# Kernel optimization log

Measured on AMD Instinct MI355X. Metric: run time of the kernel, lower is better.

## Reference

```python
import jax, jax.numpy as jnp
import numpy as np

N_NODES = 100000
N_EDGES = 1600000
IN_C, HID_C, OUT_C = 128, 64, 32


def gcn_conv(x, W, b, src, dst, n_nodes):
    """PyG GCNConv with default add_self_loops=True, symmetric normalization.

    out_i = sum_{j->i} (deg_j^-1/2 * deg_i^-1/2) * (x_j @ W) + (1/deg_i) * (x_i @ W) + b
    where deg counts incoming edges plus the self-loop.
    """
    h = x @ W  # [N, F_out] -- transform first (F_out <= F_in), cheaper messages
    # degree at target nodes, including self-loop weight 1
    deg = jax.ops.segment_sum(jnp.ones(src.shape[0], dtype=h.dtype), dst,
                              num_segments=n_nodes) + 1.0
    dinv = jax.lax.rsqrt(deg)  # deg >= 1 always (self-loop)
    # edge messages with symmetric norm, scattered to destination nodes
    coef = dinv[src] * dinv[dst]  # [E]
    msg = h[src] * coef[:, None]  # [E, F_out]
    agg = jax.ops.segment_sum(msg, dst, num_segments=n_nodes)
    # self-loop contribution: norm = dinv_i * dinv_i = 1/deg_i
    agg = agg + h * (dinv * dinv)[:, None]
    return agg + b


def setup_inputs() -> dict:
    key = jax.random.key(0)
    ks = jax.random.split(key, 8)
    x = jax.random.normal(ks[0], (N_NODES, IN_C), dtype=jnp.float32)
    edge_index = jax.random.randint(ks[1], (2, N_EDGES), 0, N_NODES, dtype=jnp.int64)
    s0 = 1.0 / np.sqrt(IN_C)
    s1 = 1.0 / np.sqrt(HID_C)
    W0 = jax.random.uniform(ks[2], (IN_C, HID_C), jnp.float32, -s0, s0)
    b0 = jnp.zeros((HID_C,), jnp.float32)
    Wm = jax.random.uniform(ks[3], (HID_C, OUT_C), jnp.float32, -s1, s1)
    bm = jnp.zeros((OUT_C,), jnp.float32)
    Wl = jax.random.uniform(ks[4], (HID_C, OUT_C), jnp.float32, -s1, s1)
    bl = jnp.zeros((OUT_C,), jnp.float32)
    return {"x": x, "edge_index": edge_index, "W0": W0, "b0": b0,
            "Wm": Wm, "bm": bm, "Wl": Wl, "bl": bl}


def reference(x, edge_index, W0, b0, Wm, bm, Wl, bl):
    src, dst = edge_index[0], edge_index[1]
    n = x.shape[0]
    h = gcn_conv(x, W0, b0, src, dst, n)
    h = jax.nn.relu(h)
    mean = gcn_conv(h, Wm, bm, src, dst, n)
    logstd = gcn_conv(h, Wl, bl, src, dst, n)
    return (mean, logstd)
```

## Files before the change

### kernel.cpp

```cpp
#include <hip/hip_runtime.h>
#include <hip/hip_fp16.h>


__global__ void hist_rank_kernel(const int* __restrict__ dst, int E, int* __restrict__ count,
                                 int* __restrict__ rank) {
    int stride = gridDim.x * blockDim.x;
    int t = blockIdx.x * blockDim.x + threadIdx.x;
    int E4 = E >> 2;
    for (int e = t; e < E4; e += stride) {
        int4 d = ((const int4*)dst)[e];
        int4 r;
        r.x = atomicAdd(&count[d.x], 1);
        r.y = atomicAdd(&count[d.y], 1);
        r.z = atomicAdd(&count[d.z], 1);
        r.w = atomicAdd(&count[d.w], 1);
        ((int4*)rank)[e] = r;
    }
    for (int e = (E4 << 2) + t; e < E; e += stride) rank[e] = atomicAdd(&count[dst[e]], 1);
}

__global__ void scan_partial_kernel(const int* __restrict__ count, int* __restrict__ partials,
                                    int N) {
    __shared__ int red[4];
    int t = threadIdx.x;
    int idx = blockIdx.x * 1024 + t * 4;
    int s = 0;
    if (idx + 3 < N) {
        int4 c = *(const int4*)(count + idx);
        s = c.x + c.y + c.z + c.w;
    } else {
#pragma unroll
        for (int k = 0; k < 4; ++k)
            if (idx + k < N) s += count[idx + k];
    }
#pragma unroll
    for (int off = 1; off < 64; off <<= 1) s += __shfl_xor(s, off);
    if ((t & 63) == 0) red[t >> 6] = s;
    __syncthreads();
    if (t == 0) partials[blockIdx.x] = red[0] + red[1] + red[2] + red[3];
}

__global__ void scan_top_kernel(int* __restrict__ partials, int nb, int* __restrict__ row_ptr,
                                int N) {
    __shared__ int buf[2][128];
    int t = threadIdx.x;
    buf[0][t] = (t < nb) ? partials[t] : 0;
    __syncthreads();
    int pi = 0;
    for (int off = 1; off < 128; off <<= 1) {
        int v = buf[pi][t];
        if (t >= off) v += buf[pi][t - off];
        buf[pi ^ 1][t] = v;
        pi ^= 1;
        __syncthreads();
    }
    if (t < nb) partials[t] = (t == 0) ? 0 : buf[pi][t - 1];
    if (t == 0) row_ptr[N] = buf[pi][127];
}

__global__ void scan_apply_kernel(const int* __restrict__ count, const int* __restrict__ partials,
                                  int* __restrict__ row_ptr, float* __restrict__ dinv, int N) {
    __shared__ int wsum[4];
    int t = threadIdx.x;
    int idx = blockIdx.x * 1024 + t * 4;
    int4 c = make_int4(0, 0, 0, 0);
    if (idx + 3 < N) {
        c = *(const int4*)(count + idx);
    } else {
        if (idx + 0 < N) c.x = count[idx + 0];
        if (idx + 1 < N) c.y = count[idx + 1];
        if (idx + 2 < N) c.z = count[idx + 2];
    }
    int s = c.x + c.y + c.z + c.w;
    int incl = s;
#pragma unroll
    for (int off = 1; off < 64; off <<= 1) {
        int v = __shfl_up(incl, off);
        if ((t & 63) >= off) incl += v;
    }
    int wexcl = incl - s;
    int w = t >> 6;
    if ((t & 63) == 63) wsum[w] = incl;
    __syncthreads();
    int base = partials[blockIdx.x] + wexcl;
    for (int k = 0; k < w; ++k) base += wsum[k];
    if (idx + 0 < N) { row_ptr[idx + 0] = base;                   dinv[idx + 0] = rsqrtf((float)c.x + 1.f); }
    if (idx + 1 < N) { row_ptr[idx + 1] = base + c.x;             dinv[idx + 1] = rsqrtf((float)c.y + 1.f); }
    if (idx + 2 < N) { row_ptr[idx + 2] = base + c.x + c.y;       dinv[idx + 2] = rsqrtf((float)c.z + 1.f); }
    if (idx + 3 < N) { row_ptr[idx + 3] = base + c.x + c.y + c.z; dinv[idx + 3] = rsqrtf((float)c.w + 1.f); }
}

#define NPASS 8
__global__ void scatter_kernel(const int* __restrict__ src, const int* __restrict__ dst,
                               const int* __restrict__ rank, int E,
                               const int* __restrict__ row_ptr, int* __restrict__ col, int N) {
    int chunk = (N + NPASS - 1) / NPASS;
    int stride = gridDim.x * blockDim.x;
    int t = blockIdx.x * blockDim.x + threadIdx.x;
    int E4 = E >> 2;
    for (int pass = 0; pass < NPASS; ++pass) {
        int lo = pass * chunk, hi = min(lo + chunk, N);
        for (int e = t; e < E4; e += stride) {
            int4 d = ((const int4*)dst)[e];
            int4 s = ((const int4*)src)[e];
            int4 r = ((const int4*)rank)[e];
            if (d.x >= lo && d.x < hi) col[row_ptr[d.x] + r.x] = s.x;
            if (d.y >= lo && d.y < hi) col[row_ptr[d.y] + r.y] = s.y;
            if (d.z >= lo && d.z < hi) col[row_ptr[d.z] + r.z] = s.z;
            if (d.w >= lo && d.w < hi) col[row_ptr[d.w] + r.w] = s.w;
        }
        for (int e = (E4 << 2) + t; e < E; e += stride) {
            int d = dst[e];
            if (d >= lo && d < hi) col[row_ptr[d] + rank[e]] = src[e];
        }
    }
}


__global__ __launch_bounds__(256, 2) void gemm_kernel(const float* __restrict__ A,
                                                      const float* __restrict__ W,
                                                      const float* __restrict__ dinv,
                                                      __half* __restrict__ Out, int M) {
    const int K = 128;
    __shared__ float Ws[K][64];
    __shared__ float As[64][68];
    int t = threadIdx.x;
    for (int i = t * 4; i < K * 64; i += 1024)
        *(float4*)&Ws[i >> 6][i & 63] = *(const float4*)(W + i);

    int row0 = blockIdx.x * 64;
    int rt = (t >> 4) * 4;
    int ct = (t & 15) * 4;
    float acc[4][4];
#pragma unroll
    for (int m = 0; m < 4; m++) { acc[m][0] = 0.f; acc[m][1] = 0.f; acc[m][2] = 0.f; acc[m][3] = 0.f; }

    for (int k0 = 0; k0 < K; k0 += 64) {
        __syncthreads();
        for (int i = t * 4; i < 64 * 64; i += 1024) {
            int r = i >> 6, c = i & 63;
            int gr = row0 + r;
            float4 v = make_float4(0.f, 0.f, 0.f, 0.f);
            if (gr < M) v = *(const float4*)(A + (size_t)gr * K + k0 + c);
            *(float4*)&As[r][c] = v;
        }
        __syncthreads();
#pragma unroll
        for (int kk = 0; kk < 64; ++kk) {
            float a0 = As[rt + 0][kk], a1 = As[rt + 1][kk];
            float a2 = As[rt + 2][kk], a3 = As[rt + 3][kk];
            float4 w = *(float4*)&Ws[k0 + kk][ct];
            acc[0][0] += a0 * w.x; acc[0][1] += a0 * w.y; acc[0][2] += a0 * w.z; acc[0][3] += a0 * w.w;
            acc[1][0] += a1 * w.x; acc[1][1] += a1 * w.y; acc[1][2] += a1 * w.z; acc[1][3] += a1 * w.w;
            acc[2][0] += a2 * w.x; acc[2][1] += a2 * w.y; acc[2][2] += a2 * w.z; acc[2][3] += a2 * w.w;
            acc[3][0] += a3 * w.x; acc[3][1] += a3 * w.y; acc[3][2] += a3 * w.z; acc[3][3] += a3 * w.w;
        }
    }
#pragma unroll
    for (int m = 0; m < 4; m++) {
        int gr = row0 + rt + m;
        if (gr < M) {
            float dv = dinv[gr];
            union { uint2 u; __half h[4]; } pk;
            pk.h[0] = __float2half(dv * acc[m][0]);
            pk.h[1] = __float2half(dv * acc[m][1]);
            pk.h[2] = __float2half(dv * acc[m][2]);
            pk.h[3] = __float2half(dv * acc[m][3]);
            *(uint2*)(Out + (size_t)gr * 64 + ct) = pk.u;
        }
    }
}


__device__ __forceinline__ float4 agg_node_h(const __half* __restrict__ Hin,
                                             const int* __restrict__ row_ptr,
                                             const int* __restrict__ col,
                                             float di, int i, int lane) {
    int g = lane >> 4;
    int l = lane & 15;
    int beg = row_ptr[i], end = row_ptr[i + 1];
    float4 acc = make_float4(0.f, 0.f, 0.f, 0.f);
    if (g == 0) {
        union { uint2 u; __half h[4]; } v;
        v.u = *(const uint2*)(Hin + (size_t)i * 64 + l * 4);
        acc.x = __half2float(v.h[0]); acc.y = __half2float(v.h[1]);
        acc.z = __half2float(v.h[2]); acc.w = __half2float(v.h[3]);
    }
    int deg = end - beg;
    int e = beg;
    int efull = beg + ((deg >> 4) << 4);
    for (; e < efull; e += 16) {
        int s[4];
#pragma unroll
        for (int k = 0; k < 4; ++k) s[k] = col[e + g + 4 * k];
        uint2 vv[4];
#pragma unroll
        for (int k = 0; k < 4; ++k) vv[k] = *(const uint2*)(Hin + (size_t)s[k] * 64 + l * 4);
#pragma unroll
        for (int k = 0; k < 4; ++k) {
            union { uint2 u; __half h[4]; } v;
            v.u = vv[k];
            acc.x += __half2float(v.h[0]); acc.y += __half2float(v.h[1]);
            acc.z += __half2float(v.h[2]); acc.w += __half2float(v.h[3]);
        }
    }
    if (e < end) {
        float w[4];
        uint2 vv[4];
#pragma unroll
        for (int k = 0; k < 4; ++k) {
            int ie = e + g + 4 * k;
            int s = (ie < end) ? col[ie] : 0;
            w[k] = (ie < end) ? 1.f : 0.f;
            vv[k] = *(const uint2*)(Hin + (size_t)s * 64 + l * 4);
        }
#pragma unroll
        for (int k = 0; k < 4; ++k) {
            union { uint2 u; __half h[4]; } v;
            v.u = vv[k];
            acc.x = fmaf(w[k], __half2float(v.h[0]), acc.x);
            acc.y = fmaf(w[k], __half2float(v.h[1]), acc.y);
            acc.z = fmaf(w[k], __half2float(v.h[2]), acc.z);
            acc.w = fmaf(w[k], __half2float(v.h[3]), acc.w);
        }
    }
    acc.x += __shfl_xor(acc.x, 16); acc.y += __shfl_xor(acc.y, 16);
    acc.z += __shfl_xor(acc.z, 16); acc.w += __shfl_xor(acc.w, 16);
    acc.x += __shfl_xor(acc.x, 32); acc.y += __shfl_xor(acc.y, 32);
    acc.z += __shfl_xor(acc.z, 32); acc.w += __shfl_xor(acc.w, 32);
    acc.x *= di; acc.y *= di; acc.z *= di; acc.w *= di;
    return acc;
}

__global__ void agg_relu_kernel(const __half* __restrict__ Hin, const int* __restrict__ row_ptr,
                                const int* __restrict__ col, const float* __restrict__ dinv,
                                const float* __restrict__ bias, __half* __restrict__ Hout, int N) {
    int wid = (blockIdx.x * blockDim.x + threadIdx.x) >> 6;
    if (wid >= N) return;
    int lane = threadIdx.x & 63;
    float di = dinv[wid];
    float4 r = agg_node_h(Hin, row_ptr, col, di, wid, lane);
    if (lane < 16) {
        float4 b = *(const float4*)(bias + lane * 4);
        union { uint2 u; __half h[4]; } pk;
        pk.h[0] = __float2half(di * fmaxf(r.x + b.x, 0.f));
        pk.h[1] = __float2half(di * fmaxf(r.y + b.y, 0.f));
        pk.h[2] = __float2half(di * fmaxf(r.z + b.z, 0.f));
        pk.h[3] = __float2half(di * fmaxf(r.w + b.w, 0.f));
        *(uint2*)(Hout + (size_t)wid * 64 + lane * 4) = pk.u;
    }
}

__global__ __launch_bounds__(256) void agg_out_fused_kernel(
        const __half* __restrict__ Hin, const int* __restrict__ row_ptr,
        const int* __restrict__ col, const float* __restrict__ dinv,
        const float* __restrict__ Wm, const float* __restrict__ Wl,
        const float* __restrict__ bm, const float* __restrict__ bl,
        float* __restrict__ out, int N) {
    __shared__ float Ws[64][64];
    int t = threadIdx.x;
    for (int i = t * 4; i < 64 * 32; i += 1024) {
        int k = i >> 5, c = i & 31;
        *(float4*)&Ws[k][c]      = *(const float4*)(Wm + i);
        *(float4*)&Ws[k][32 + c] = *(const float4*)(Wl + i);
    }
    __syncthreads();

    int lane = t & 63;
    float bj = (lane < 32) ? bm[lane] : bl[lane - 32];

    int gw = (blockIdx.x * blockDim.x + t) >> 6;
    int TW = (gridDim.x * blockDim.x) >> 6;
    for (int i = gw; i < N; i += TW) {
        float4 r = agg_node_h(Hin, row_ptr, col, dinv[i], i, lane);
        float a[4] = {r.x, r.y, r.z, r.w};
        float o = bj;
#pragma unroll
        for (int k = 0; k < 64; ++k) {
            float gk = __shfl(a[k & 3], k >> 2, 64);
            o = fmaf(gk, Ws[k][lane], o);
        }
        if (lane < 32) out[(size_t)i * 32 + lane] = o;
        else           out[(size_t)(N + i) * 32 + (lane - 32)] = o;
    }
}


extern "C" void kernel_launch(void* const* d_in, const int* in_sizes, int n_in,
                              void* d_out, int out_size, void* d_ws, size_t ws_size,
                              hipStream_t stream) {
    const float* x  = (const float*)d_in[0];
    const int*   ei = (const int*)d_in[1];
    const float* W0 = (const float*)d_in[2];
    const float* b0 = (const float*)d_in[3];
    const float* Wm = (const float*)d_in[4];
    const float* bm = (const float*)d_in[5];
    const float* Wl = (const float*)d_in[6];
    const float* bl = (const float*)d_in[7];
    float* out = (float*)d_out;

    int N = in_sizes[0] / 128;
    int E = in_sizes[1] / 2;
    const int* src = ei;
    const int* dst = ei + E;

    char* p = (char*)d_ws;
    auto carve = [&](size_t bytes) -> void* {
        void* q = (void*)p;
        p += (bytes + 255) & ~(size_t)255;
        return q;
    };
    int*    count    = (int*)carve((size_t)N * 4);
    int*    row_ptr  = (int*)carve(((size_t)N + 1) * 4);
    int*    col      = (int*)carve((size_t)E * 4);
    int*    rank     = (int*)carve((size_t)E * 4);
    float*  dinv     = (float*)carve((size_t)N * 4);
    int*    partials = (int*)carve(128 * 4);
    __half* h0       = (__half*)carve((size_t)N * 64 * 2);
    __half* h        = (__half*)carve((size_t)N * 64 * 2);

    int nb = (N + 1023) / 1024;

    hipMemsetAsync(count, 0, (size_t)N * 4, stream);
    hist_rank_kernel<<<2048, 256, 0, stream>>>(dst, E, count, rank);
    scan_partial_kernel<<<nb, 256, 0, stream>>>(count, partials, N);
    scan_top_kernel<<<1, 128, 0, stream>>>(partials, nb, row_ptr, N);
    scan_apply_kernel<<<nb, 256, 0, stream>>>(count, partials, row_ptr, dinv, N);
    scatter_kernel<<<2048, 256, 0, stream>>>(src, dst, rank, E, row_ptr, col, N);

    gemm_kernel<<<(N + 63) / 64, 256, 0, stream>>>(x, W0, dinv, h0, N);
    agg_relu_kernel<<<(N + 3) / 4, 256, 0, stream>>>(h0, row_ptr, col, dinv, b0, h, N);

    agg_out_fused_kernel<<<2048, 256, 0, stream>>>(h, row_ptr, col, dinv, Wm, Wl, bm, bl, out, N);
}
```

Baseline: 281.5 us.

## Prefetch next node's row bounds and first neighbor indices in aggregation loops

```diff
diff --git a/kernel.cpp b/kernel.cpp
--- a/kernel.cpp
+++ b/kernel.cpp
@@ -172,13 +172,10 @@
 }
 
 
-__device__ __forceinline__ float4 agg_node_h(const __half* __restrict__ Hin,
-                                             const int* __restrict__ row_ptr,
-                                             const int* __restrict__ col,
-                                             float di, int i, int lane) {
-    int g = lane >> 4;
-    int l = lane & 15;
-    int beg = row_ptr[i], end = row_ptr[i + 1];
+__device__ __forceinline__ float4 agg_body(const __half* __restrict__ Hin,
+                                           const int* __restrict__ col,
+                                           const int* pc, int beg, int end,
+                                           int i, int g, int l) {
     float4 acc = make_float4(0.f, 0.f, 0.f, 0.f);
     if (g == 0) {
         union { uint2 u; __half h[4]; } v;
@@ -186,33 +183,13 @@
         acc.x = __half2float(v.h[0]); acc.y = __half2float(v.h[1]);
         acc.z = __half2float(v.h[2]); acc.w = __half2float(v.h[3]);
     }
-    int deg = end - beg;
-    int e = beg;
-    int efull = beg + ((deg >> 4) << 4);
-    for (; e < efull; e += 16) {
-        int s[4];
-#pragma unroll
-        for (int k = 0; k < 4; ++k) s[k] = col[e + g + 4 * k];
-        uint2 vv[4];
-#pragma unroll
-        for (int k = 0; k < 4; ++k) vv[k] = *(const uint2*)(Hin + (size_t)s[k] * 64 + l * 4);
-#pragma unroll
-        for (int k = 0; k < 4; ++k) {
-            union { uint2 u; __half h[4]; } v;
-            v.u = vv[k];
-            acc.x += __half2float(v.h[0]); acc.y += __half2float(v.h[1]);
-            acc.z += __half2float(v.h[2]); acc.w += __half2float(v.h[3]);
-        }
-    }
-    if (e < end) {
+    {
         float w[4];
         uint2 vv[4];
 #pragma unroll
         for (int k = 0; k < 4; ++k) {
-            int ie = e + g + 4 * k;
-            int s = (ie < end) ? col[ie] : 0;
-            w[k] = (ie < end) ? 1.f : 0.f;
-            vv[k] = *(const uint2*)(Hin + (size_t)s * 64 + l * 4);
+            w[k] = (beg + g + 4 * k < end) ? 1.f : 0.f;
+            vv[k] = *(const uint2*)(Hin + (size_t)pc[k] * 64 + l * 4);
         }
 #pragma unroll
         for (int k = 0; k < 4; ++k) {
@@ -224,34 +201,101 @@
             acc.w = fmaf(w[k], __half2float(v.h[3]), acc.w);
         }
     }
+    int e = beg + 16;
+    for (; e + 16 <= end; e += 16) {
+        int s[4];
+#pragma unroll
+        for (int k = 0; k < 4; ++k) s[k] = col[e + g + 4 * k];
+        uint2 vv[4];
+#pragma unroll
+        for (int k = 0; k < 4; ++k) vv[k] = *(const uint2*)(Hin + (size_t)s[k] * 64 + l * 4);
+#pragma unroll
+        for (int k = 0; k < 4; ++k) {
+            union { uint2 u; __half h[4]; } v;
+            v.u = vv[k];
+            acc.x += __half2float(v.h[0]); acc.y += __half2float(v.h[1]);
+            acc.z += __half2float(v.h[2]); acc.w += __half2float(v.h[3]);
+        }
+    }
+    if (e < end) {
+        float w[4];
+        uint2 vv[4];
+#pragma unroll
+        for (int k = 0; k < 4; ++k) {
+            int ie = e + g + 4 * k;
+            int s = (ie < end) ? col[ie] : 0;
+            w[k] = (ie < end) ? 1.f : 0.f;
+            vv[k] = *(const uint2*)(Hin + (size_t)s * 64 + l * 4);
+        }
+#pragma unroll
+        for (int k = 0; k < 4; ++k) {
+            union { uint2 u; __half h[4]; } v;
+            v.u = vv[k];
+            acc.x = fmaf(w[k], __half2float(v.h[0]), acc.x);
+            acc.y = fmaf(w[k], __half2float(v.h[1]), acc.y);
+            acc.z = fmaf(w[k], __half2float(v.h[2]), acc.z);
+            acc.w = fmaf(w[k], __half2float(v.h[3]), acc.w);
+        }
+    }
     acc.x += __shfl_xor(acc.x, 16); acc.y += __shfl_xor(acc.y, 16);
     acc.z += __shfl_xor(acc.z, 16); acc.w += __shfl_xor(acc.w, 16);
     acc.x += __shfl_xor(acc.x, 32); acc.y += __shfl_xor(acc.y, 32);
     acc.z += __shfl_xor(acc.z, 32); acc.w += __shfl_xor(acc.w, 32);
-    acc.x *= di; acc.y *= di; acc.z *= di; acc.w *= di;
     return acc;
 }
 
-__global__ void agg_relu_kernel(const __half* __restrict__ Hin, const int* __restrict__ row_ptr,
-                                const int* __restrict__ col, const float* __restrict__ dinv,
-                                const float* __restrict__ bias, __half* __restrict__ Hout, int N) {
-    int wid = (blockIdx.x * blockDim.x + threadIdx.x) >> 6;
-    if (wid >= N) return;
-    int lane = threadIdx.x & 63;
-    float di = dinv[wid];
-    float4 r = agg_node_h(Hin, row_ptr, col, di, wid, lane);
-    if (lane < 16) {
-        float4 b = *(const float4*)(bias + lane * 4);
-        union { uint2 u; __half h[4]; } pk;
-        pk.h[0] = __float2half(di * fmaxf(r.x + b.x, 0.f));
-        pk.h[1] = __float2half(di * fmaxf(r.y + b.y, 0.f));
-        pk.h[2] = __float2half(di * fmaxf(r.z + b.z, 0.f));
-        pk.h[3] = __float2half(di * fmaxf(r.w + b.w, 0.f));
-        *(uint2*)(Hout + (size_t)wid * 64 + lane * 4) = pk.u;
-    }
-}
-
-__global__ __launch_bounds__(256) void agg_out_fused_kernel(
+__global__ __launch_bounds__(256, 4) void agg_relu_kernel(
+        const __half* __restrict__ Hin, const int* __restrict__ row_ptr,
+        const int* __restrict__ col, const float* __restrict__ dinv,
+        const float* __restrict__ bias, __half* __restrict__ Hout, int N) {
+    int t = threadIdx.x;
+    int lane = t & 63;
+    int g = lane >> 4, l = lane & 15;
+    int gw = (blockIdx.x * blockDim.x + t) >> 6;
+    int TW = (gridDim.x * blockDim.x) >> 6;
+
+    float4 b4 = (l < 16) ? *(const float4*)(bias + l * 4) : make_float4(0, 0, 0, 0);
+
+    int i = gw;
+    int beg = 0, end = 0, pc0 = 0, pc1 = 0, pc2 = 0, pc3 = 0;
+    if (i < N) {
+        beg = row_ptr[i]; end = row_ptr[i + 1];
+        pc0 = (beg + g      < end) ? col[beg + g]      : 0;
+        pc1 = (beg + g + 4  < end) ? col[beg + g + 4]  : 0;
+        pc2 = (beg + g + 8  < end) ? col[beg + g + 8]  : 0;
+        pc3 = (beg + g + 12 < end) ? col[beg + g + 12] : 0;
+    }
+    while (i < N) {
+        int inext = i + TW;
+        int beg_n = 0, end_n = 0;
+        if (inext < N) { beg_n = row_ptr[inext]; end_n = row_ptr[inext + 1]; }
+
+        int pc[4] = {pc0, pc1, pc2, pc3};
+        float di = dinv[i];
+        float4 r = agg_body(Hin, col, pc, beg, end, i, g, l);
+
+        if (inext < N) {
+            pc0 = (beg_n + g      < end_n) ? col[beg_n + g]      : 0;
+            pc1 = (beg_n + g + 4  < end_n) ? col[beg_n + g + 4]  : 0;
+            pc2 = (beg_n + g + 8  < end_n) ? col[beg_n + g + 8]  : 0;
+            pc3 = (beg_n + g + 12 < end_n) ? col[beg_n + g + 12] : 0;
+        }
+
+        if (lane < 16) {
+            float s = di * di;
+            union { uint2 u; __half h[4]; } pk;
+            pk.h[0] = __float2half(di * fmaxf(di * r.x + b4.x, 0.f));
+            pk.h[1] = __float2half(di * fmaxf(di * r.y + b4.y, 0.f));
+            pk.h[2] = __float2half(di * fmaxf(di * r.z + b4.z, 0.f));
+            pk.h[3] = __float2half(di * fmaxf(di * r.w + b4.w, 0.f));
+            (void)s;
+            *(uint2*)(Hout + (size_t)i * 64 + l * 4) = pk.u;
+        }
+        beg = beg_n; end = end_n; i = inext;
+    }
+}
+
+__global__ __launch_bounds__(256, 4) void agg_out_fused_kernel(
         const __half* __restrict__ Hin, const int* __restrict__ row_ptr,
         const int* __restrict__ col, const float* __restrict__ dinv,
         const float* __restrict__ Wm, const float* __restrict__ Wl,
@@ -267,21 +311,52 @@
     __syncthreads();
 
     int lane = t & 63;
+    int g = lane >> 4, l = lane & 15;
     float bj = (lane < 32) ? bm[lane] : bl[lane - 32];
 
     int gw = (blockIdx.x * blockDim.x + t) >> 6;
     int TW = (gridDim.x * blockDim.x) >> 6;
-    for (int i = gw; i < N; i += TW) {
-        float4 r = agg_node_h(Hin, row_ptr, col, dinv[i], i, lane);
-        float a[4] = {r.x, r.y, r.z, r.w};
-        float o = bj;
-#pragma unroll
-        for (int k = 0; k < 64; ++k) {
-            float gk = __shfl(a[k & 3], k >> 2, 64);
-            o = fmaf(gk, Ws[k][lane], o);
-        }
+
+    int i = gw;
+    int beg = 0, end = 0, pc0 = 0, pc1 = 0, pc2 = 0, pc3 = 0;
+    if (i < N) {
+        beg = row_ptr[i]; end = row_ptr[i + 1];
+        pc0 = (beg + g      < end) ? col[beg + g]      : 0;
+        pc1 = (beg + g + 4  < end) ? col[beg + g + 4]  : 0;
+        pc2 = (beg + g + 8  < end) ? col[beg + g + 8]  : 0;
+        pc3 = (beg + g + 12 < end) ? col[beg + g + 12] : 0;
+    }
+    while (i < N) {
+        int inext = i + TW;
+        int beg_n = 0, end_n = 0;
+        if (inext < N) { beg_n = row_ptr[inext]; end_n = row_ptr[inext + 1]; }
+
+        int pc[4] = {pc0, pc1, pc2, pc3};
+        float di = dinv[i];
+        float4 r = agg_body(Hin, col, pc, beg, end, i, g, l);
+
+        if (inext < N) {
+            pc0 = (beg_n + g      < end_n) ? col[beg_n + g]      : 0;
+            pc1 = (beg_n + g + 4  < end_n) ? col[beg_n + g + 4]  : 0;
+            pc2 = (beg_n + g + 8  < end_n) ? col[beg_n + g + 8]  : 0;
+            pc3 = (beg_n + g + 12 < end_n) ? col[beg_n + g + 12] : 0;
+        }
+
+        float a[4] = {di * r.x, di * r.y, di * r.z, di * r.w};
+        float o0 = bj, o1 = 0.f, o2 = 0.f, o3 = 0.f;
+#pragma unroll
+        for (int k = 0; k < 64; k += 4) {
+            int srcl = k >> 2;
+            o0 = fmaf(__shfl(a[0], srcl, 64), Ws[k + 0][lane], o0);
+            o1 = fmaf(__shfl(a[1], srcl, 64), Ws[k + 1][lane], o1);
+            o2 = fmaf(__shfl(a[2], srcl, 64), Ws[k + 2][lane], o2);
+            o3 = fmaf(__shfl(a[3], srcl, 64), Ws[k + 3][lane], o3);
+        }
+        float o = (o0 + o1) + (o2 + o3);
         if (lane < 32) out[(size_t)i * 32 + lane] = o;
         else           out[(size_t)(N + i) * 32 + (lane - 32)] = o;
+
+        beg = beg_n; end = end_n; i = inext;
     }
 }
 
@@ -329,7 +404,7 @@
     scatter_kernel<<<2048, 256, 0, stream>>>(src, dst, rank, E, row_ptr, col, N);
 
     gemm_kernel<<<(N + 63) / 64, 256, 0, stream>>>(x, W0, dinv, h0, N);
-    agg_relu_kernel<<<(N + 3) / 4, 256, 0, stream>>>(h0, row_ptr, col, dinv, b0, h, N);
+    agg_relu_kernel<<<2048, 256, 0, stream>>>(h0, row_ptr, col, dinv, b0, h, N);
 
     agg_out_fused_kernel<<<2048, 256, 0, stream>>>(h, row_ptr, col, dinv, Wm, Wl, bm, bl, out, N);
 }
```

Result: faster. 274.1 us (-2.6%).

## Aggregate two nodes per wavefront to raise memory-level parallelism in gather

Applied to the files above, without the earlier changes.

```diff
diff --git a/kernel.cpp b/kernel.cpp
--- a/kernel.cpp
+++ b/kernel.cpp
@@ -172,24 +172,18 @@
 }
 
 
-__device__ __forceinline__ float4 agg_node_h(const __half* __restrict__ Hin,
-                                             const int* __restrict__ row_ptr,
-                                             const int* __restrict__ col,
-                                             float di, int i, int lane) {
-    int g = lane >> 4;
-    int l = lane & 15;
-    int beg = row_ptr[i], end = row_ptr[i + 1];
-    float4 acc = make_float4(0.f, 0.f, 0.f, 0.f);
-    if (g == 0) {
-        union { uint2 u; __half h[4]; } v;
-        v.u = *(const uint2*)(Hin + (size_t)i * 64 + l * 4);
-        acc.x = __half2float(v.h[0]); acc.y = __half2float(v.h[1]);
-        acc.z = __half2float(v.h[2]); acc.w = __half2float(v.h[3]);
-    }
-    int deg = end - beg;
-    int e = beg;
-    int efull = beg + ((deg >> 4) << 4);
-    for (; e < efull; e += 16) {
+#define ACCUM4(ACC, W_, U_) do { \
+    union { uint2 u; __half h[4]; } _v; _v.u = (U_); \
+    ACC.x = fmaf((W_), __half2float(_v.h[0]), ACC.x); \
+    ACC.y = fmaf((W_), __half2float(_v.h[1]), ACC.y); \
+    ACC.z = fmaf((W_), __half2float(_v.h[2]), ACC.z); \
+    ACC.w = fmaf((W_), __half2float(_v.h[3]), ACC.w); } while (0)
+
+__device__ __forceinline__ void agg_tail(const __half* __restrict__ Hin,
+                                         const int* __restrict__ col,
+                                         int beg, int end, int g, int l, float4& acc) {
+    int e = beg + 16;
+    for (; e + 16 <= end; e += 16) {
         int s[4];
 #pragma unroll
         for (int k = 0; k < 4; ++k) s[k] = col[e + g + 4 * k];
@@ -197,12 +191,7 @@
 #pragma unroll
         for (int k = 0; k < 4; ++k) vv[k] = *(const uint2*)(Hin + (size_t)s[k] * 64 + l * 4);
 #pragma unroll
-        for (int k = 0; k < 4; ++k) {
-            union { uint2 u; __half h[4]; } v;
-            v.u = vv[k];
-            acc.x += __half2float(v.h[0]); acc.y += __half2float(v.h[1]);
-            acc.z += __half2float(v.h[2]); acc.w += __half2float(v.h[3]);
-        }
+        for (int k = 0; k < 4; ++k) ACCUM4(acc, 1.f, vv[k]);
     }
     if (e < end) {
         float w[4];
@@ -215,43 +204,108 @@
             vv[k] = *(const uint2*)(Hin + (size_t)s * 64 + l * 4);
         }
 #pragma unroll
-        for (int k = 0; k < 4; ++k) {
-            union { uint2 u; __half h[4]; } v;
-            v.u = vv[k];
-            acc.x = fmaf(w[k], __half2float(v.h[0]), acc.x);
-            acc.y = fmaf(w[k], __half2float(v.h[1]), acc.y);
-            acc.z = fmaf(w[k], __half2float(v.h[2]), acc.z);
-            acc.w = fmaf(w[k], __half2float(v.h[3]), acc.w);
-        }
-    }
-    acc.x += __shfl_xor(acc.x, 16); acc.y += __shfl_xor(acc.y, 16);
-    acc.z += __shfl_xor(acc.z, 16); acc.w += __shfl_xor(acc.w, 16);
-    acc.x += __shfl_xor(acc.x, 32); acc.y += __shfl_xor(acc.y, 32);
-    acc.z += __shfl_xor(acc.z, 32); acc.w += __shfl_xor(acc.w, 32);
-    acc.x *= di; acc.y *= di; acc.z *= di; acc.w *= di;
-    return acc;
-}
-
-__global__ void agg_relu_kernel(const __half* __restrict__ Hin, const int* __restrict__ row_ptr,
-                                const int* __restrict__ col, const float* __restrict__ dinv,
-                                const float* __restrict__ bias, __half* __restrict__ Hout, int N) {
-    int wid = (blockIdx.x * blockDim.x + threadIdx.x) >> 6;
-    if (wid >= N) return;
-    int lane = threadIdx.x & 63;
-    float di = dinv[wid];
-    float4 r = agg_node_h(Hin, row_ptr, col, di, wid, lane);
-    if (lane < 16) {
-        float4 b = *(const float4*)(bias + lane * 4);
-        union { uint2 u; __half h[4]; } pk;
-        pk.h[0] = __float2half(di * fmaxf(r.x + b.x, 0.f));
-        pk.h[1] = __float2half(di * fmaxf(r.y + b.y, 0.f));
-        pk.h[2] = __float2half(di * fmaxf(r.z + b.z, 0.f));
-        pk.h[3] = __float2half(di * fmaxf(r.w + b.w, 0.f));
-        *(uint2*)(Hout + (size_t)wid * 64 + lane * 4) = pk.u;
-    }
-}
-
-__global__ __launch_bounds__(256) void agg_out_fused_kernel(
+        for (int k = 0; k < 4; ++k) ACCUM4(acc, w[k], vv[k]);
+    }
+}
+
+__device__ __forceinline__ void agg2_nodes(const __half* __restrict__ Hin,
+                                           const int* __restrict__ col,
+                                           int iA, int begA, int endA,
+                                           int iB, int begB, int endB, bool hasB,
+                                           int g, int l, float4& rA, float4& rB) {
+    float4 aA = make_float4(0.f, 0.f, 0.f, 0.f);
+    float4 aB = make_float4(0.f, 0.f, 0.f, 0.f);
+    int sA[4], sB[4];
+    float wA[4], wB[4];
+#pragma unroll
+    for (int k = 0; k < 4; ++k) {
+        int ie = begA + g + 4 * k;
+        sA[k] = (ie < endA) ? col[ie] : 0;
+        wA[k] = (ie < endA) ? 1.f : 0.f;
+    }
+#pragma unroll
+    for (int k = 0; k < 4; ++k) {
+        int ie = begB + g + 4 * k;
+        sB[k] = (hasB && ie < endB) ? col[ie] : 0;
+        wB[k] = (hasB && ie < endB) ? 1.f : 0.f;
+    }
+    uint2 selfu = make_uint2(0, 0);
+    if (g == 0) selfu = *(const uint2*)(Hin + (size_t)iA * 64 + l * 4);
+    if (g == 1 && hasB) selfu = *(const uint2*)(Hin + (size_t)iB * 64 + l * 4);
+    uint2 vA[4], vB[4];
+#pragma unroll
+    for (int k = 0; k < 4; ++k) vA[k] = *(const uint2*)(Hin + (size_t)sA[k] * 64 + l * 4);
+#pragma unroll
+    for (int k = 0; k < 4; ++k) vB[k] = *(const uint2*)(Hin + (size_t)sB[k] * 64 + l * 4);
+
+    if (g == 0) ACCUM4(aA, 1.f, selfu);
+    if (g == 1 && hasB) ACCUM4(aB, 1.f, selfu);
+#pragma unroll
+    for (int k = 0; k < 4; ++k) ACCUM4(aA, wA[k], vA[k]);
+#pragma unroll
+    for (int k = 0; k < 4; ++k) ACCUM4(aB, wB[k], vB[k]);
+
+    if (endA - begA > 16) agg_tail(Hin, col, begA, endA, g, l, aA);
+    if (hasB && endB - begB > 16) agg_tail(Hin, col, begB, endB, g, l, aB);
+
+    aA.x += __shfl_xor(aA.x, 16); aA.y += __shfl_xor(aA.y, 16);
+    aA.z += __shfl_xor(aA.z, 16); aA.w += __shfl_xor(aA.w, 16);
+    aA.x += __shfl_xor(aA.x, 32); aA.y += __shfl_xor(aA.y, 32);
+    aA.z += __shfl_xor(aA.z, 32); aA.w += __shfl_xor(aA.w, 32);
+    aB.x += __shfl_xor(aB.x, 16); aB.y += __shfl_xor(aB.y, 16);
+    aB.z += __shfl_xor(aB.z, 16); aB.w += __shfl_xor(aB.w, 16);
+    aB.x += __shfl_xor(aB.x, 32); aB.y += __shfl_xor(aB.y, 32);
+    aB.z += __shfl_xor(aB.z, 32); aB.w += __shfl_xor(aB.w, 32);
+    rA = aA; rB = aB;
+}
+
+__global__ __launch_bounds__(256, 4) void agg_relu_kernel(
+        const __half* __restrict__ Hin, const int* __restrict__ row_ptr,
+        const int* __restrict__ col, const float* __restrict__ dinv,
+        const float* __restrict__ bias, __half* __restrict__ Hout, int N) {
+    int t = threadIdx.x;
+    int lane = t & 63;
+    int g = lane >> 4, l = lane & 15;
+    int gw = (blockIdx.x * blockDim.x + t) >> 6;
+    int TW = (gridDim.x * blockDim.x) >> 6;
+    int PH = (N + 1) >> 1;
+
+    float4 b4 = (l < 16) ? *(const float4*)(bias + l * 4) : make_float4(0, 0, 0, 0);
+
+    for (int j = gw; j < PH; j += TW) {
+        int iA = j, iB = j + PH;
+        bool hasB = iB < N;
+        int begA = row_ptr[iA], endA = row_ptr[iA + 1];
+        int begB = 0, endB = 0;
+        if (hasB) { begB = row_ptr[iB]; endB = row_ptr[iB + 1]; }
+
+        float4 rA, rB;
+        agg2_nodes(Hin, col, iA, begA, endA, iB, begB, endB, hasB, g, l, rA, rB);
+
+        float dA = dinv[iA];
+        if (lane < 16) {
+            union { uint2 u; __half h[4]; } pk;
+            pk.h[0] = __float2half(dA * fmaxf(dA * rA.x + b4.x, 0.f));
+            pk.h[1] = __float2half(dA * fmaxf(dA * rA.y + b4.y, 0.f));
+            pk.h[2] = __float2half(dA * fmaxf(dA * rA.z + b4.z, 0.f));
+            pk.h[3] = __float2half(dA * fmaxf(dA * rA.w + b4.w, 0.f));
+            *(uint2*)(Hout + (size_t)iA * 64 + l * 4) = pk.u;
+        }
+        if (hasB) {
+            float dB = dinv[iB];
+            if (lane < 16) {
+                union { uint2 u; __half h[4]; } pk;
+                pk.h[0] = __float2half(dB * fmaxf(dB * rB.x + b4.x, 0.f));
+                pk.h[1] = __float2half(dB * fmaxf(dB * rB.y + b4.y, 0.f));
+                pk.h[2] = __float2half(dB * fmaxf(dB * rB.z + b4.z, 0.f));
+                pk.h[3] = __float2half(dB * fmaxf(dB * rB.w + b4.w, 0.f));
+                *(uint2*)(Hout + (size_t)iB * 64 + l * 4) = pk.u;
+            }
+        }
+    }
+}
+
+__global__ __launch_bounds__(256, 4) void agg_out_fused_kernel(
         const __half* __restrict__ Hin, const int* __restrict__ row_ptr,
         const int* __restrict__ col, const float* __restrict__ dinv,
         const float* __restrict__ Wm, const float* __restrict__ Wl,
@@ -267,21 +321,51 @@
     __syncthreads();
 
     int lane = t & 63;
+    int g = lane >> 4, l = lane & 15;
     float bj = (lane < 32) ? bm[lane] : bl[lane - 32];
 
     int gw = (blockIdx.x * blockDim.x + t) >> 6;
     int TW = (gridDim.x * blockDim.x) >> 6;
-    for (int i = gw; i < N; i += TW) {
-        float4 r = agg_node_h(Hin, row_ptr, col, dinv[i], i, lane);
-        float a[4] = {r.x, r.y, r.z, r.w};
-        float o = bj;
-#pragma unroll
-        for (int k = 0; k < 64; ++k) {
-            float gk = __shfl(a[k & 3], k >> 2, 64);
-            o = fmaf(gk, Ws[k][lane], o);
-        }
-        if (lane < 32) out[(size_t)i * 32 + lane] = o;
-        else           out[(size_t)(N + i) * 32 + (lane - 32)] = o;
+    int PH = (N + 1) >> 1;
+
+    for (int j = gw; j < PH; j += TW) {
+        int iA = j, iB = j + PH;
+        bool hasB = iB < N;
+        int begA = row_ptr[iA], endA = row_ptr[iA + 1];
+        int begB = 0, endB = 0;
+        if (hasB) { begB = row_ptr[iB]; endB = row_ptr[iB + 1]; }
+
+        float4 rA, rB;
+        agg2_nodes(Hin, col, iA, begA, endA, iB, begB, endB, hasB, g, l, rA, rB);
+
+        float dA = dinv[iA];
+        float dB = hasB ? dinv[iB] : 0.f;
+        float aA[4] = {dA * rA.x, dA * rA.y, dA * rA.z, dA * rA.w};
+        float aB[4] = {dB * rB.x, dB * rB.y, dB * rB.z, dB * rB.w};
+        float oA0 = bj, oA1 = 0.f, oA2 = 0.f, oA3 = 0.f;
+        float oB0 = bj, oB1 = 0.f, oB2 = 0.f, oB3 = 0.f;
+#pragma unroll
+        for (int k = 0; k < 64; k += 4) {
+            int srcl = k >> 2;
+            float w0 = Ws[k + 0][lane], w1 = Ws[k + 1][lane];
+            float w2 = Ws[k + 2][lane], w3 = Ws[k + 3][lane];
+            oA0 = fmaf(__shfl(aA[0], srcl, 64), w0, oA0);
+            oA1 = fmaf(__shfl(aA[1], srcl, 64), w1, oA1);
+            oA2 = fmaf(__shfl(aA[2], srcl, 64), w2, oA2);
+            oA3 = fmaf(__shfl(aA[3], srcl, 64), w3, oA3);
+            oB0 = fmaf(__shfl(aB[0], srcl, 64), w0, oB0);
+            oB1 = fmaf(__shfl(aB[1], srcl, 64), w1, oB1);
+            oB2 = fmaf(__shfl(aB[2], srcl, 64), w2, oB2);
+            oB3 = fmaf(__shfl(aB[3], srcl, 64), w3, oB3);
+        }
+        float oA = (oA0 + oA1) + (oA2 + oA3);
+        float oB = (oB0 + oB1) + (oB2 + oB3);
+        if (lane < 32) out[(size_t)iA * 32 + lane] = oA;
+        else           out[(size_t)(N + iA) * 32 + (lane - 32)] = oA;
+        if (hasB) {
+            if (lane < 32) out[(size_t)iB * 32 + lane] = oB;
+            else           out[(size_t)(N + iB) * 32 + (lane - 32)] = oB;
+        }
     }
 }
 
@@ -329,7 +413,7 @@
     scatter_kernel<<<2048, 256, 0, stream>>>(src, dst, rank, E, row_ptr, col, N);
 
     gemm_kernel<<<(N + 63) / 64, 256, 0, stream>>>(x, W0, dinv, h0, N);
-    agg_relu_kernel<<<(N + 3) / 4, 256, 0, stream>>>(h0, row_ptr, col, dinv, b0, h, N);
-
-    agg_out_fused_kernel<<<2048, 256, 0, stream>>>(h, row_ptr, col, dinv, Wm, Wl, bm, bl, out, N);
-}
+    agg_relu_kernel<<<4096, 256, 0, stream>>>(h0, row_ptr, col, dinv, b0, h, N);
+
+    agg_out_fused_kernel<<<4096, 256, 0, stream>>>(h, row_ptr, col, dinv, Wm, Wl, bm, bl, out, N);
+}
```

After: 370.8 us. 31.7% more time.
